# Optimization experiments

Measured on AMD Instinct MI355X. Metric: run time of the kernel, lower is better.

## Reference

```python
import jax, jax.numpy as jnp
import numpy as np

DN = ('NCHW', 'OIHW', 'NCHW')

def conv2d(x, w, b):
    y = jax.lax.conv_general_dilated(x, w, (1, 1), 'SAME', dimension_numbers=DN)
    return y + b[None, :, None, None]

def deform_conv2d(x, offset, w, b):
    # torchvision DeformConv2d v1: kernel 3x3, stride 1, pad 1, dilation 1, no mask.
    # offset: [B, 18, H, W] ordered (dy0, dx0, dy1, dx1, ...) over row-major kernel taps.
    B, C, H, W = x.shape
    K2 = 9
    ki = (jnp.arange(K2) // 3).astype(x.dtype)  # kernel row index i
    kj = (jnp.arange(K2) % 3).astype(x.dtype)   # kernel col index j
    dy = offset[:, 0::2]  # [B, 9, H, W]
    dx = offset[:, 1::2]
    hh = jnp.arange(H, dtype=x.dtype)
    ww = jnp.arange(W, dtype=x.dtype)
    # sampling positions: p = out_pos - pad + k + offset
    py = hh[None, None, :, None] + ki[None, :, None, None] - 1.0 + dy  # [B,9,H,W]
    px = ww[None, None, None, :] + kj[None, :, None, None] - 1.0 + dx

    xf = x.reshape(B, C, H * W)
    y0 = jnp.floor(py); x0 = jnp.floor(px)
    y1 = y0 + 1.0;      x1 = x0 + 1.0
    wy1 = py - y0; wy0 = 1.0 - wy1
    wx1 = px - x0; wx0 = 1.0 - wx1

    def corner(yc, xc, cw):
        valid = (yc >= 0) & (yc <= H - 1) & (xc >= 0) & (xc <= W - 1)
        yi = jnp.clip(yc, 0, H - 1).astype(jnp.int32)
        xi = jnp.clip(xc, 0, W - 1).astype(jnp.int32)
        idx = yi * W + xi                       # [B,9,H,W]
        v = jax.vmap(lambda img, i: img[:, i])(xf, idx)  # [B,C,9,H,W]
        return v * (cw * valid.astype(x.dtype))[:, None]

    sampled = (corner(y0, x0, wy0 * wx0) + corner(y0, x1, wy0 * wx1)
               + corner(y1, x0, wy1 * wx0) + corner(y1, x1, wy1 * wx1))  # [B,C,9,H,W]
    out = jnp.einsum('bckhw,ock->bohw', sampled, w.reshape(w.shape[0], C, K2))
    return out + b[None, :, None, None]

def setup_inputs() -> dict:
    key = jax.random.key(0)
    ks = jax.random.split(key, 20)
    B, C, H, W = 8, 64, 128, 128
    O = 64
    s = 0.05
    inp = {
        'x': jax.random.normal(ks[0], (B, C, H, W), jnp.float32),
        'bsize': jax.random.uniform(ks[1], (B, 2), jnp.float32),
        # glob: Linear(2,64) -> ReLU -> Linear(64,32)
        'gw1': s * jax.random.normal(ks[2], (64, 2), jnp.float32),
        'gb1': jnp.zeros((64,), jnp.float32),
        'gw2': s * jax.random.normal(ks[3], (32, 64), jnp.float32),
        'gb2': jnp.zeros((32,), jnp.float32),
        # local: Conv2d(C,32,3) -> ReLU -> Conv2d(32,32,3)
        'lw1': s * jax.random.normal(ks[4], (32, C, 3, 3), jnp.float32),
        'lb1': jnp.zeros((32,), jnp.float32),
        'lw2': s * jax.random.normal(ks[5], (32, 32, 3, 3), jnp.float32),
        'lb2': jnp.zeros((32,), jnp.float32),
        # fuse: Conv2d(64,32,3) -> ReLU -> Conv2d(32,18,3)
        'fw1': s * jax.random.normal(ks[6], (32, 64, 3, 3), jnp.float32),
        'fb1': jnp.zeros((32,), jnp.float32),
        'fw2': s * jax.random.normal(ks[7], (18, 32, 3, 3), jnp.float32),
        'fb2': jnp.zeros((18,), jnp.float32),
        # deformable conv weight (copied from the source nn.Conv2d) + its own bias
        'dw': s * jax.random.normal(ks[8], (O, C, 3, 3), jnp.float32),
        'db': jnp.zeros((O,), jnp.float32),
    }
    return inp

def reference(x, bsize, gw1, gb1, gw2, gb2, lw1, lb1, lw2, lb2,
              fw1, fb1, fw2, fb2, dw, db):
    B, C, H, W = x.shape
    # global branch: MLP on box-size -> broadcast over spatial dims
    g = jax.nn.relu(bsize @ gw1.T + gb1) @ gw2.T + gb2          # [B,32]
    g_offset = jnp.broadcast_to(g[:, :, None, None], (B, 32, H, W))
    # local branch
    l_offset = conv2d(jax.nn.relu(conv2d(x, lw1, lb1)), lw2, lb2)  # [B,32,H,W]
    # fuse -> 18 offset channels
    fused = jnp.concatenate((g_offset, l_offset), axis=1)          # [B,64,H,W]
    offset = conv2d(jax.nn.relu(conv2d(fused, fw1, fb1)), fw2, fb2)  # [B,18,H,W]
    fea = deform_conv2d(x, offset, dw, db)
    return jax.nn.relu(fea)
```

## Files before the change

kernel.cpp:

```cpp
#include <hip/hip_runtime.h>

#define BB 8
#define CC 64
#define HH 128
#define WW 128
#define HWSZ (HH*WW)

typedef _Float16 h16;
typedef __attribute__((ext_vector_type(8))) _Float16 h16x8;
typedef __attribute__((ext_vector_type(4))) _Float16 h16x4;
typedef __attribute__((ext_vector_type(2))) _Float16 h16x2;
typedef __attribute__((ext_vector_type(4))) float f32x4;

typedef const __attribute__((address_space(1))) unsigned int* gptr_t;
typedef __attribute__((address_space(3))) unsigned int* lptr_t;

__device__ __forceinline__ void conv_pack(int j, int NCG, const float* w,
                                          int maxo, h16* dst) {
  int e = j & 7, l4 = (j >> 3) & 3, l15 = (j >> 5) & 15, f = (j >> 9) & 1;
  int cg = (j >> 10) & (NCG - 1), kt = (j >> 10) / NCG;
  int o = f * 16 + l15, c = cg * 32 + l4 * 8 + e;
  int CINw = NCG * 32;
  dst[j] = (o < maxo) ? (h16)w[(o * CINw + c) * 9 + kt] : (h16)0.f;
}

__global__ __launch_bounds__(256) void prep_kernel(
    const float* __restrict__ bsize, const float* __restrict__ gw1,
    const float* __restrict__ gb1, const float* __restrict__ gw2,
    const float* __restrict__ gb2, float* __restrict__ g,
    const float* __restrict__ lw1, const float* __restrict__ lw2,
    const float* __restrict__ fw1, const float* __restrict__ fw2,
    const float* __restrict__ dw, h16* __restrict__ cwq,
    h16* __restrict__ dwq, const float* __restrict__ x,
    h16* __restrict__ xt) {
  __shared__ float hbuf[BB][64];
  const int blk = blockIdx.x;
  const int tid = threadIdx.x;
  if (blk == 0) {
#pragma unroll
    for (int i2 = 0; i2 < 2; ++i2) {
      int idx = i2 * 256 + tid;
      int b = idx >> 6, i = idx & 63;
      float v = fmaf(bsize[b * 2 + 0], gw1[i * 2 + 0],
                     fmaf(bsize[b * 2 + 1], gw1[i * 2 + 1], gb1[i]));
      hbuf[b][i] = fmaxf(v, 0.f);
    }
    __syncthreads();
    int b = tid >> 5, j = tid & 31;
    float acc = gb2[j];
#pragma unroll
    for (int i = 0; i < 64; ++i) acc = fmaf(hbuf[b][i], gw2[j * 64 + i], acc);
    g[b * 32 + j] = acc;
  } else if (blk <= 360) {
    int i = (blk - 1) * 256 + tid;
    if (i < 18432) {
      conv_pack(i, 2, lw1, 32, cwq);
    } else if (i < 27648) {
      conv_pack(i - 18432, 1, lw2, 32, cwq + 18432);
    } else if (i < 46080) {
      conv_pack(i - 27648, 2, fw1, 32, cwq + 27648);
    } else if (i < 55296) {
      conv_pack(i - 46080, 1, fw2, 18, cwq + 46080);
    } else if (i < 55296 + 36864) {
      int j = i - 55296;
      int e = j & 7, l4 = (j >> 3) & 3, l15 = (j >> 5) & 15;
      int og = (j >> 9) & 3, cg = (j >> 11) & 1, kt = j >> 12;
      int o = og * 16 + l15, c = cg * 32 + l4 * 8 + e;
      dwq[j] = (h16)dw[(o * 64 + c) * 9 + kt];
    }
  } else {
    int j = blk - 361;
    int b = (1 + j) & 7;
    int slot = j >> 3;
    int t = b * 16384 + slot * 256 + tid;
    int p = t & 16383;
    const float* xb = x + (size_t)b * 64 * HWSZ + p;
    h16* ob = xt + (size_t)t * 64;
#pragma unroll
    for (int c0 = 0; c0 < 64; c0 += 8) {
      h16x8 v;
#pragma unroll
      for (int i = 0; i < 8; ++i) v[i] = (h16)xb[(size_t)(c0 + i) * HWSZ];
      *(h16x8*)(ob + c0) = v;
    }
  }
}

template <int NCG, bool GFUSE, bool RELU, int OMODE>
__global__ __launch_bounds__(512) void conv_mfma_kernel(
    const h16* __restrict__ in, const h16* __restrict__ cwq,
    const float* __restrict__ bias, const float* __restrict__ g,
    h16* __restrict__ outv) {
  constexpr int CINS = GFUSE ? 32 : NCG * 32;
  constexpr int NS = CINS / 8;
  constexpr int LOG2NS = (NS == 8) ? 3 : 2;
  constexpr int NCHUNK = 4 * 128 * NS;
  __shared__ __align__(16) h16 sh[4 * 128 * CINS];
  const int wgid = (blockIdx.x & 7) * 64 + (blockIdx.x >> 3);
  const int b = wgid >> 6;
  const int h0 = (wgid & 63) * 2;
  const int lane = threadIdx.x & 63, wave = threadIdx.x >> 6;
  const int wr = wave >> 2, wv = wave & 3;
  const int h = h0 + wr;
  const int l15 = lane & 15, l4 = lane >> 4;
  const h16* inb = in + (size_t)b * HWSZ * CINS;

#pragma unroll
  for (int it = 0; it < NCHUNK / 512; ++it) {
    int q = it * 512 + threadIdx.x;
    int sp = q & (NS - 1), pr = q >> LOG2NS;
    int r = pr >> 7, px = pr & 127;
    int gy = min(max(h0 - 1 + r, 0), HH - 1);
    int s = sp ^ (px & (NS - 1));
    const h16* src = inb + ((size_t)gy * WW + px) * CINS + s * 8;
    __builtin_amdgcn_global_load_lds(
        (gptr_t)src, (lptr_t)(sh + (size_t)(it * 512 + wave * 64) * 8), 16, 0, 0);
  }

  const h16x8 zfr = {0, 0, 0, 0, 0, 0, 0, 0};
  h16x8 gfr = zfr;
  if (GFUSE) {
#pragma unroll
    for (int i = 0; i < 8; ++i) gfr[i] = (h16)g[b * 32 + l4 * 8 + i];
  }
  __syncthreads();

  f32x4 acc[2][2];
#pragma unroll
  for (int f = 0; f < 2; ++f)
#pragma unroll
    for (int j = 0; j < 2; ++j) acc[f][j] = (f32x4){0.f, 0.f, 0.f, 0.f};

#pragma unroll
  for (int kt = 0; kt < 9; ++kt) {
    const int ki = kt / 3 - 1, kj = kt % 3 - 1;
    const int y = h + ki;
    const bool yok = (unsigned)y < HH;
    const int r = ki + 1 + wr;
    int xs[2];
    bool ok[2];
#pragma unroll
    for (int j = 0; j < 2; ++j) {
      int xx = wv * 32 + j * 16 + l15 + kj;
      ok[j] = yok && ((unsigned)xx < WW);
      xs[j] = min(max(xx, 0), WW - 1);
    }
#pragma unroll
    for (int cg = 0; cg < NCG; ++cg) {
      const h16* aq = cwq + (size_t)((kt * NCG + cg) * 2) * 512 + l15 * 32 + l4 * 8;
      h16x8 afr0 = *(const h16x8*)(aq);
      h16x8 afr1 = *(const h16x8*)(aq + 512);
#pragma unroll
      for (int j = 0; j < 2; ++j) {
        h16x8 bv;
        if (GFUSE && cg == 0) {
          bv = ok[j] ? gfr : zfr;
        } else {
          const int s = (!GFUSE && NCG == 2) ? cg * 4 + l4 : l4;
          h16x8 ld = *(const h16x8*)(sh + (r * 128 + xs[j]) * CINS +
                                     ((s ^ (xs[j] & (NS - 1))) * 8));
          bv = ok[j] ? ld : zfr;
        }
        acc[0][j] = __builtin_amdgcn_mfma_f32_16x16x32_f16(afr0, bv, acc[0][j], 0, 0, 0);
        acc[1][j] = __builtin_amdgcn_mfma_f32_16x16x32_f16(afr1, bv, acc[1][j], 0, 0, 0);
      }
    }
  }
  if (OMODE == 0) {
    h16* ob = outv + (size_t)b * HWSZ * 32;
#pragma unroll
    for (int f = 0; f < 2; ++f)
#pragma unroll
      for (int j = 0; j < 2; ++j) {
        int p = h * WW + wv * 32 + j * 16 + l15;
        int o0 = f * 16 + l4 * 4;
        h16x4 st;
#pragma unroll
        for (int r2 = 0; r2 < 4; ++r2) {
          float v = acc[f][j][r2] + bias[o0 + r2];
          if (RELU) v = fmaxf(v, 0.f);
          st[r2] = (h16)v;
        }
        *(h16x4*)(ob + (size_t)p * 32 + o0) = st;
      }
  } else {
    h16* ob = outv + (size_t)b * HWSZ * 24;
#pragma unroll
    for (int j = 0; j < 2; ++j) {
      int p = h * WW + wv * 32 + j * 16 + l15;
      {
        int o0 = l4 * 4;
        h16x4 st;
#pragma unroll
        for (int r2 = 0; r2 < 4; ++r2) st[r2] = (h16)(acc[0][j][r2] + bias[o0 + r2]);
        *(h16x4*)(ob + (size_t)p * 24 + o0) = st;
      }
      if (l4 == 0) {
        h16x2 st2;
        st2[0] = (h16)(acc[1][j][0] + bias[16]);
        st2[1] = (h16)(acc[1][j][1] + bias[17]);
        *(h16x2*)(ob + (size_t)p * 24 + 16) = st2;
      }
    }
  }
}

__global__ __launch_bounds__(128) void deform_mfma_kernel(
    const h16* __restrict__ xt, const h16* __restrict__ offc,
    const h16* __restrict__ dwq, const float* __restrict__ db,
    float* __restrict__ out) {
  __shared__ __align__(16) h16 sh[5 * 40 * 64];
  const int wgid = (blockIdx.x & 7) * 512 + (blockIdx.x >> 3);
  const int b = wgid >> 9;
  const int rh = wgid & 511;
  const int h = rh >> 2;
  const int qx = (rh & 3) * 32;
  const int x_lo = qx - 4;
  const int lane = threadIdx.x & 63, wave = threadIdx.x >> 6;
  const int l15 = lane & 15, l4 = lane >> 4;
  const int wx = qx + wave * 16;
  const int p0 = h * WW + wx;
  const int myw = wx + l15;
  const int mypix = p0 + l15;
  const h16* xb = xt + (size_t)b * HWSZ * 64;

#pragma unroll
  for (int it = 0; it < 13; ++it) {
    int q = it * 128 + threadIdx.x;
    if (q < 1600) {
      int sp = q & 7, pr = q >> 3;
      int r = pr / 40, i = pr - r * 40;
      int gy = min(max(h - 2 + r, 0), HH - 1);
      int gx = min(max(x_lo + i, 0), WW - 1);
      int s = sp ^ (i & 7);
      const h16* src = xb + ((size_t)gy * WW + gx) * 64 + s * 8;
      __builtin_amdgcn_global_load_lds(
          (gptr_t)src, (lptr_t)(sh + (size_t)(it * 128 + wave * 64) * 8), 16, 0, 0);
    }
  }

  const h16* offp = offc + ((size_t)b * HWSZ + mypix) * 24;
  h16x8 offv0 = *(const h16x8*)(offp);
  h16x8 offv1 = *(const h16x8*)(offp + 8);
  h16x8 offv2 = *(const h16x8*)(offp + 16);
  __syncthreads();

#define OFFE(e) ((e) < 8 ? (float)offv0[(e) & 7] : (e) < 16 ? (float)offv1[(e) & 7] : (float)offv2[(e) & 7])

  f32x4 acc[4];
#pragma unroll
  for (int og = 0; og < 4; ++og) acc[og] = (f32x4){0.f, 0.f, 0.f, 0.f};

  h16x8 pc[2][2][4];
  h16x8 pw[2][8];
  h16   pg[2][4];

#define PREF(kt, par) do {                                                  \
    float py = (float)(h + (kt) / 3 - 1) + OFFE(2 * (kt));                  \
    float px = (float)(myw + (kt) % 3 - 1) + OFFE(2 * (kt) + 1);            \
    float y0f = floorf(py), x0f = floorf(px);                               \
    float wy1 = py - y0f, wy0 = 1.f - wy1;                                  \
    float wx1 = px - x0f, wx0 = 1.f - wx1;                                  \
    int y0 = (int)y0f, x0i = (int)x0f;                                      \
    int y1 = y0 + 1, x1i = x0i + 1;                                         \
    bool y0ok = (unsigned)y0 < HH, y1ok = (unsigned)y1 < HH;                \
    bool x0ok = (unsigned)x0i < WW, x1ok = (unsigned)x1i < WW;              \
    pg[par][0] = (h16)((y0ok && x0ok) ? wy0 * wx0 : 0.f);                   \
    pg[par][1] = (h16)((y0ok && x1ok) ? wy0 * wx1 : 0.f);                   \
    pg[par][2] = (h16)((y1ok && x0ok) ? wy1 * wx0 : 0.f);                   \
    pg[par][3] = (h16)((y1ok && x1ok) ? wy1 * wx1 : 0.f);                   \
    int y0c = min(max(y0, 0), HH - 1), y1c = min(max(y1, 0), HH - 1);       \
    int x0c = min(max(x0i, 0), WW - 1), x1c = min(max(x1i, 0), WW - 1);     \
    int ty0u = y0c - (h - 2), ty1u = y1c - (h - 2);                         \
    int tx0u = x0c - x_lo, tx1u = x1c - x_lo;                               \
    bool fast = ((unsigned)ty0u <= 4u) & ((unsigned)ty1u <= 4u) &           \
                ((unsigned)tx0u <= 39u) & ((unsigned)tx1u <= 39u);          \
    int ty0 = min(max(ty0u, 0), 4), ty1 = min(max(ty1u, 0), 4);             \
    int tx0 = min(max(tx0u, 0), 39), tx1 = min(max(tx1u, 0), 39);           \
    int pr00 = (ty0 * 40 + tx0) * 64, pr01 = (ty0 * 40 + tx1) * 64;         \
    int pr10 = (ty1 * 40 + tx0) * 64, pr11 = (ty1 * 40 + tx1) * 64;         \
    int sx0 = (tx0 & 7) * 8, sx1 = (tx1 & 7) * 8;                           \
    _Pragma("unroll")                                                       \
    for (int cg = 0; cg < 2; ++cg) {                                        \
      int sb = (cg * 4 + l4) * 8;                                           \
      pc[par][cg][0] = *(const h16x8*)(sh + pr00 + (sb ^ sx0));             \
      pc[par][cg][1] = *(const h16x8*)(sh + pr01 + (sb ^ sx1));             \
      pc[par][cg][2] = *(const h16x8*)(sh + pr10 + (sb ^ sx0));             \
      pc[par][cg][3] = *(const h16x8*)(sh + pr11 + (sb ^ sx1));             \
    }                                                                       \
    if (!fast) {                                                            \
      int i00 = y0c * WW + x0c, i01 = y0c * WW + x1c;                       \
      int i10 = y1c * WW + x0c, i11 = y1c * WW + x1c;                       \
      _Pragma("unroll")                                                     \
      for (int cg = 0; cg < 2; ++cg) {                                      \
        const h16* cb = xb + cg * 32 + l4 * 8;                              \
        pc[par][cg][0] = *(const h16x8*)(cb + (size_t)i00 * 64);            \
        pc[par][cg][1] = *(const h16x8*)(cb + (size_t)i01 * 64);            \
        pc[par][cg][2] = *(const h16x8*)(cb + (size_t)i10 * 64);            \
        pc[par][cg][3] = *(const h16x8*)(cb + (size_t)i11 * 64);            \
      }                                                                     \
    }                                                                       \
    const h16* wq0 = dwq + ((size_t)((kt) * 2 + 0) * 64 + l15) * 32 + l4 * 8; \
    const h16* wq1 = dwq + ((size_t)((kt) * 2 + 1) * 64 + l15) * 32 + l4 * 8; \
    pw[par][0] = *(const h16x8*)(wq0 + 0 * 512);                            \
    pw[par][1] = *(const h16x8*)(wq0 + 1 * 512);                            \
    pw[par][2] = *(const h16x8*)(wq0 + 2 * 512);                            \
    pw[par][3] = *(const h16x8*)(wq0 + 3 * 512);                            \
    pw[par][4] = *(const h16x8*)(wq1 + 0 * 512);                            \
    pw[par][5] = *(const h16x8*)(wq1 + 1 * 512);                            \
    pw[par][6] = *(const h16x8*)(wq1 + 2 * 512);                            \
    pw[par][7] = *(const h16x8*)(wq1 + 3 * 512);                            \
  } while (0)

#define CONS(par) do {                                                      \
    h16 w00 = pg[par][0], w01 = pg[par][1], w10 = pg[par][2], w11 = pg[par][3]; \
    h16x8 s0 = pc[par][0][0] * w00 + pc[par][0][1] * w01                    \
             + pc[par][0][2] * w10 + pc[par][0][3] * w11;                   \
    h16x8 s1 = pc[par][1][0] * w00 + pc[par][1][1] * w01                    \
             + pc[par][1][2] * w10 + pc[par][1][3] * w11;                   \
    acc[0] = __builtin_amdgcn_mfma_f32_16x16x32_f16(s0, pw[par][0], acc[0], 0, 0, 0); \
    acc[1] = __builtin_amdgcn_mfma_f32_16x16x32_f16(s0, pw[par][1], acc[1], 0, 0, 0); \
    acc[2] = __builtin_amdgcn_mfma_f32_16x16x32_f16(s0, pw[par][2], acc[2], 0, 0, 0); \
    acc[3] = __builtin_amdgcn_mfma_f32_16x16x32_f16(s0, pw[par][3], acc[3], 0, 0, 0); \
    acc[0] = __builtin_amdgcn_mfma_f32_16x16x32_f16(s1, pw[par][4], acc[0], 0, 0, 0); \
    acc[1] = __builtin_amdgcn_mfma_f32_16x16x32_f16(s1, pw[par][5], acc[1], 0, 0, 0); \
    acc[2] = __builtin_amdgcn_mfma_f32_16x16x32_f16(s1, pw[par][6], acc[2], 0, 0, 0); \
    acc[3] = __builtin_amdgcn_mfma_f32_16x16x32_f16(s1, pw[par][7], acc[3], 0, 0, 0); \
  } while (0)

  PREF(0, 0);
  PREF(1, 1);
  CONS(0);
  PREF(2, 0);
  CONS(1);
  PREF(3, 1);
  CONS(0);
  PREF(4, 0);
  CONS(1);
  PREF(5, 1);
  CONS(0);
  PREF(6, 0);
  CONS(1);
  PREF(7, 1);
  CONS(0);
  PREF(8, 0);
  CONS(1);
  CONS(0);
#undef PREF
#undef CONS
#undef OFFE

  float* outb = out + (size_t)b * CC * HWSZ;
#pragma unroll
  for (int og = 0; og < 4; ++og) {
    int o = og * 16 + l15;
    float bv = db[o];
    f32x4 st;
#pragma unroll
    for (int r = 0; r < 4; ++r) st[r] = fmaxf(acc[og][r] + bv, 0.f);
    *(f32x4*)(outb + (size_t)o * HWSZ + p0 + l4 * 4) = st;
  }
}

extern "C" void kernel_launch(void* const* d_in, const int* in_sizes, int n_in,
                              void* d_out, int out_size, void* d_ws, size_t ws_size,
                              hipStream_t stream) {
  const float* x     = (const float*)d_in[0];
  const float* bsize = (const float*)d_in[1];
  const float* gw1   = (const float*)d_in[2];
  const float* gb1   = (const float*)d_in[3];
  const float* gw2   = (const float*)d_in[4];
  const float* gb2   = (const float*)d_in[5];
  const float* lw1   = (const float*)d_in[6];
  const float* lb1   = (const float*)d_in[7];
  const float* lw2   = (const float*)d_in[8];
  const float* lb2   = (const float*)d_in[9];
  const float* fw1   = (const float*)d_in[10];
  const float* fb1   = (const float*)d_in[11];
  const float* fw2   = (const float*)d_in[12];
  const float* fb2   = (const float*)d_in[13];
  const float* dw    = (const float*)d_in[14];
  const float* db    = (const float*)d_in[15];
  float* out = (float*)d_out;

  float* gbuf = (float*)d_ws;
  h16* xt   = (h16*)((char*)d_ws + 2048);
  h16* offc = (h16*)((char*)d_ws + 2048 + (size_t)BB * HWSZ * 64 * 2);
  h16* dwq  = (h16*)((char*)offc + (size_t)BB * HWSZ * 24 * 2);

  h16* loff = (h16*)d_out;
  h16* cwq  = (h16*)d_out + 4194304;
  h16* t12  = (h16*)d_out + 8388608;
  const h16* lw1q = cwq;
  const h16* lw2q = cwq + 18432;
  const h16* fw1q = cwq + 27648;
  const h16* fw2q = cwq + 46080;

  prep_kernel<<<873, 256, 0, stream>>>(bsize, gw1, gb1, gw2, gb2, gbuf,
                                       lw1, lw2, fw1, fw2, dw, cwq, dwq, x, xt);
  conv_mfma_kernel<2, false, true, 0><<<512, 512, 0, stream>>>(
      xt, lw1q, lb1, nullptr, t12);
  conv_mfma_kernel<1, false, false, 0><<<512, 512, 0, stream>>>(
      t12, lw2q, lb2, nullptr, loff);
  conv_mfma_kernel<2, true, true, 0><<<512, 512, 0, stream>>>(
      loff, fw1q, fb1, gbuf, t12);
  conv_mfma_kernel<1, false, false, 1><<<512, 512, 0, stream>>>(
      t12, fw2q, fb2, nullptr, offc);
  deform_mfma_kernel<<<4096, 128, 0, stream>>>(xt, offc, dwq, db, out);
}
```

Measured before the change: 101.7 us.

## Process two tiles per deform block with double-buffered LDS staging

The deform kernel now handles two adjacent 32-pixel row segments per workgroup. It issues the async global-to-LDS load for the second tile's input patch before computing the first tile, so the load overlaps with the first tile's compute. Grid size is halved and shared memory per block doubles. The two tiles are horizontally adjacent in the same row, so their staged halos overlap but are still loaded twice. The larger LDS footprint may lower occupancy.

```diff
diff --git a/kernel.cpp b/kernel.cpp
--- a/kernel.cpp
+++ b/kernel.cpp
@@ -209,51 +209,53 @@
     const h16* __restrict__ xt, const h16* __restrict__ offc,
     const h16* __restrict__ dwq, const float* __restrict__ db,
     float* __restrict__ out) {
-  __shared__ __align__(16) h16 sh[5 * 40 * 64];
-  const int wgid = (blockIdx.x & 7) * 512 + (blockIdx.x >> 3);
-  const int b = wgid >> 9;
-  const int rh = wgid & 511;
-  const int h = rh >> 2;
-  const int qx = (rh & 3) * 32;
-  const int x_lo = qx - 4;
+  __shared__ __align__(16) h16 sh[2 * 5 * 40 * 64];
+  const int wgid = (blockIdx.x & 7) * 256 + (blockIdx.x >> 3);
+  const int b = wgid >> 8;
+  const int pair = wgid & 255;
   const int lane = threadIdx.x & 63, wave = threadIdx.x >> 6;
   const int l15 = lane & 15, l4 = lane >> 4;
-  const int wx = qx + wave * 16;
-  const int p0 = h * WW + wx;
-  const int myw = wx + l15;
-  const int mypix = p0 + l15;
   const h16* xb = xt + (size_t)b * HWSZ * 64;
 
-#pragma unroll
-  for (int it = 0; it < 13; ++it) {
-    int q = it * 128 + threadIdx.x;
-    if (q < 1600) {
-      int sp = q & 7, pr = q >> 3;
-      int r = pr / 40, i = pr - r * 40;
-      int gy = min(max(h - 2 + r, 0), HH - 1);
-      int gx = min(max(x_lo + i, 0), WW - 1);
-      int s = sp ^ (i & 7);
-      const h16* src = xb + ((size_t)gy * WW + gx) * 64 + s * 8;
-      __builtin_amdgcn_global_load_lds(
-          (gptr_t)src, (lptr_t)(sh + (size_t)(it * 128 + wave * 64) * 8), 16, 0, 0);
-    }
-  }
-
-  const h16* offp = offc + ((size_t)b * HWSZ + mypix) * 24;
-  h16x8 offv0 = *(const h16x8*)(offp);
-  h16x8 offv1 = *(const h16x8*)(offp + 8);
-  h16x8 offv2 = *(const h16x8*)(offp + 16);
+#define STAGE(rh, SB) do {                                                  \
+    int h_ = (rh) >> 2, xlo_ = ((rh) & 3) * 32 - 4;                         \
+    _Pragma("unroll")                                                       \
+    for (int it = 0; it < 13; ++it) {                                       \
+      int q = it * 128 + threadIdx.x;                                       \
+      if (q < 1600) {                                                       \
+        int sp = q & 7, pr = q >> 3;                                        \
+        int r = pr / 40, i = pr - r * 40;                                   \
+        int gy = min(max(h_ - 2 + r, 0), HH - 1);                           \
+        int gx = min(max(xlo_ + i, 0), WW - 1);                             \
+        int s = sp ^ (i & 7);                                               \
+        const h16* src = xb + ((size_t)gy * WW + gx) * 64 + s * 8;          \
+        __builtin_amdgcn_global_load_lds(                                   \
+            (gptr_t)src, (lptr_t)((SB) + (size_t)(it * 128 + wave * 64) * 8), 16, 0, 0); \
+      }                                                                     \
+    }                                                                       \
+  } while (0)
+
+  const int rh0 = pair * 2, rh1 = pair * 2 + 1;
+  STAGE(rh0, sh);
+
+  h16x8 offv[2][3];
+#pragma unroll
+  for (int tt = 0; tt < 2; ++tt) {
+    int rh = pair * 2 + tt;
+    int h_ = rh >> 2, qx_ = (rh & 3) * 32;
+    int mypix = h_ * WW + qx_ + wave * 16 + l15;
+    const h16* offp = offc + ((size_t)b * HWSZ + mypix) * 24;
+    offv[tt][0] = *(const h16x8*)(offp);
+    offv[tt][1] = *(const h16x8*)(offp + 8);
+    offv[tt][2] = *(const h16x8*)(offp + 16);
+  }
   __syncthreads();
-
-#define OFFE(e) ((e) < 8 ? (float)offv0[(e) & 7] : (e) < 16 ? (float)offv1[(e) & 7] : (float)offv2[(e) & 7])
-
-  f32x4 acc[4];
-#pragma unroll
-  for (int og = 0; og < 4; ++og) acc[og] = (f32x4){0.f, 0.f, 0.f, 0.f};
 
   h16x8 pc[2][2][4];
   h16x8 pw[2][8];
   h16   pg[2][4];
+
+#define OFFE(e) ((e) < 8 ? (float)o0_[(e) & 7] : (e) < 16 ? (float)o1_[(e) & 7] : (float)o2_[(e) & 7])
 
 #define PREF(kt, par) do {                                                  \
     float py = (float)(h + (kt) / 3 - 1) + OFFE(2 * (kt));                  \
@@ -283,10 +285,10 @@
     _Pragma("unroll")                                                       \
     for (int cg = 0; cg < 2; ++cg) {                                        \
       int sb = (cg * 4 + l4) * 8;                                           \
-      pc[par][cg][0] = *(const h16x8*)(sh + pr00 + (sb ^ sx0));             \
-      pc[par][cg][1] = *(const h16x8*)(sh + pr01 + (sb ^ sx1));             \
-      pc[par][cg][2] = *(const h16x8*)(sh + pr10 + (sb ^ sx0));             \
-      pc[par][cg][3] = *(const h16x8*)(sh + pr11 + (sb ^ sx1));             \
+      pc[par][cg][0] = *(const h16x8*)(SB_ + pr00 + (sb ^ sx0));            \
+      pc[par][cg][1] = *(const h16x8*)(SB_ + pr01 + (sb ^ sx1));            \
+      pc[par][cg][2] = *(const h16x8*)(SB_ + pr10 + (sb ^ sx0));            \
+      pc[par][cg][3] = *(const h16x8*)(SB_ + pr11 + (sb ^ sx1));            \
     }                                                                       \
     if (!fast) {                                                            \
       int i00 = y0c * WW + x0c, i01 = y0c * WW + x1c;                       \
@@ -328,38 +330,58 @@
     acc[3] = __builtin_amdgcn_mfma_f32_16x16x32_f16(s1, pw[par][7], acc[3], 0, 0, 0); \
   } while (0)
 
-  PREF(0, 0);
-  PREF(1, 1);
-  CONS(0);
-  PREF(2, 0);
-  CONS(1);
-  PREF(3, 1);
-  CONS(0);
-  PREF(4, 0);
-  CONS(1);
-  PREF(5, 1);
-  CONS(0);
-  PREF(6, 0);
-  CONS(1);
-  PREF(7, 1);
-  CONS(0);
-  PREF(8, 0);
-  CONS(1);
-  CONS(0);
+#pragma unroll
+  for (int tt = 0; tt < 2; ++tt) {
+    if (tt == 0) STAGE(rh1, sh + 12800);
+    h16* SB_ = sh + tt * 12800;
+    const int rh = pair * 2 + tt;
+    const int h = rh >> 2;
+    const int qx = (rh & 3) * 32;
+    const int x_lo = qx - 4;
+    const int wx = qx + wave * 16;
+    const int p0 = h * WW + wx;
+    const int myw = wx + l15;
+    h16x8 o0_ = offv[tt][0], o1_ = offv[tt][1], o2_ = offv[tt][2];
+
+    f32x4 acc[4];
+#pragma unroll
+    for (int og = 0; og < 4; ++og) acc[og] = (f32x4){0.f, 0.f, 0.f, 0.f};
+
+    PREF(0, 0);
+    PREF(1, 1);
+    CONS(0);
+    PREF(2, 0);
+    CONS(1);
+    PREF(3, 1);
+    CONS(0);
+    PREF(4, 0);
+    CONS(1);
+    PREF(5, 1);
+    CONS(0);
+    PREF(6, 0);
+    CONS(1);
+    PREF(7, 1);
+    CONS(0);
+    PREF(8, 0);
+    CONS(1);
+    CONS(0);
+
+    float* outb = out + (size_t)b * CC * HWSZ;
+#pragma unroll
+    for (int og = 0; og < 4; ++og) {
+      int o = og * 16 + l15;
+      float bv = db[o];
+      f32x4 st;
+#pragma unroll
+      for (int r = 0; r < 4; ++r) st[r] = fmaxf(acc[og][r] + bv, 0.f);
+      *(f32x4*)(outb + (size_t)o * HWSZ + p0 + l4 * 4) = st;
+    }
+    if (tt == 0) __syncthreads();
+  }
 #undef PREF
 #undef CONS
 #undef OFFE
-
-  float* outb = out + (size_t)b * CC * HWSZ;
-#pragma unroll
-  for (int og = 0; og < 4; ++og) {
-    int o = og * 16 + l15;
-    float bv = db[o];
-    f32x4 st;
-#pragma unroll
-    for (int r = 0; r < 4; ++r) st[r] = fmaxf(acc[og][r] + bv, 0.f);
-    *(f32x4*)(outb + (size_t)o * HWSZ + p0 + l4 * 4) = st;
-  }
+#undef STAGE
 }
 
 extern "C" void kernel_launch(void* const* d_in, const int* in_sizes, int n_in,
@@ -406,5 +428,5 @@
       loff, fw1q, fb1, gbuf, t12);
   conv_mfma_kernel<1, false, false, 1><<<512, 512, 0, stream>>>(
       t12, fw2q, fb2, nullptr, offc);
-  deform_mfma_kernel<<<4096, 128, 0, stream>>>(xt, offc, dwq, db, out);
+  deform_mfma_kernel<<<2048, 128, 0, stream>>>(xt, offc, dwq, db, out);
 }
```

Measured after the change: 106.9 us. +5.2%, slower.
